# Kernel optimization log

Hardware: AMD Instinct MI355X
Metric: run time of the kernel (lower is better)

The kernel has to match this reference:

```python
import jax, jax.numpy as jnp
import numpy as np

EPS = 1e-8


def setup_inputs() -> dict:
    key = jax.random.key(0)
    k1, k2 = jax.random.split(key)
    N, D, K = 200000, 256, 64
    embeds = jax.random.normal(k1, (N, D), dtype=jnp.float32)
    init = jax.random.uniform(k2, (K, D), dtype=jnp.float32)  # torch.rand(K, n_h)
    beta = jnp.ones((1,), dtype=jnp.float32)
    return {"embeds": embeds, "init": init, "beta": beta, "num_iter": 11}


def reference(embeds, init, beta, num_iter):
    # embeds: [N, D], init: [K, D], beta: scalar temperature
    data_abs = jnp.linalg.norm(embeds, axis=1, keepdims=True)            # [N, 1]
    data_norm = embeds / jnp.maximum(data_abs, EPS)                      # [N, D]
    b = beta.reshape(())
    mu = init
    r = None
    for _ in range(num_iter):  # small fixed iteration count (default 11)
        mu_abs = jnp.linalg.norm(mu, axis=1, keepdims=True)              # [K, 1]
        mu_norm = mu / jnp.maximum(mu_abs, EPS)                          # [K, D]
        dist = data_norm @ mu_norm.T                                     # [N, K]
        r = jax.nn.softmax(b * dist, axis=1)                             # [N, K]
        cluster_r = r.sum(axis=0)                                        # [K]
        cluster_mean = r.T @ embeds                                      # [K, D]
        mu = cluster_mean / cluster_r[:, None]                           # diag(1/cluster_r) @ cluster_mean
    return mu, r
```

## Files before the change

kernel.cpp:

```cpp
#include <hip/hip_runtime.h>
#include <math.h>


#define N_ROWS 200000
#define DIM 256
#define KC 64
#define NUM_ITER 11
#define TR 64
#define NTILES (N_ROWS / TR)
#define EPSV 1e-8f
#define NB 256
#define NG2 8

typedef _Float16 half8 __attribute__((ext_vector_type(8)));
typedef _Float16 half4 __attribute__((ext_vector_type(4)));
typedef float f32x4 __attribute__((ext_vector_type(4)));

typedef __attribute__((address_space(3))) void as3_void;
typedef __attribute__((address_space(1))) void as1_void;

__device__ __forceinline__ void glds16(const void* g, void* l) {
  __builtin_amdgcn_global_load_lds((const as1_void*)g, (as3_void*)l, 16, 0, 0);
}

__device__ __forceinline__ float wave_reduce_sum(float v) {
#pragma unroll
  for (int off = 32; off > 0; off >>= 1) v += __shfl_xor(v, off, 64);
  return v;
}

__device__ __forceinline__ void barrier_lgkm_only() {
  __builtin_amdgcn_sched_barrier(0);
  asm volatile("s_waitcnt lgkmcnt(0)" ::: "memory");
  __builtin_amdgcn_s_barrier();
  __builtin_amdgcn_sched_barrier(0);
}


__global__ void rn_convert_kernel(const float* __restrict__ embeds,
                                  float* __restrict__ inv_norm,
                                  _Float16* __restrict__ Xh) {
  int gw = (blockIdx.x * blockDim.x + threadIdx.x) >> 6;
  int lane = threadIdx.x & 63;
  int nw = (gridDim.x * blockDim.x) >> 6;
  for (int row = gw; row < N_ROWS; row += nw) {
    float4 v = *(const float4*)(embeds + (size_t)row * DIM + 4 * lane);
    float s = v.x * v.x;
    s = fmaf(v.y, v.y, s); s = fmaf(v.z, v.z, s); s = fmaf(v.w, v.w, s);
    s = wave_reduce_sum(s);
    if (lane == 0) inv_norm[row] = 1.0f / fmaxf(sqrtf(s), EPSV);
    half4 h;
    h[0] = (_Float16)v.x; h[1] = (_Float16)v.y; h[2] = (_Float16)v.z; h[3] = (_Float16)v.w;
    *(half4*)(Xh + (size_t)row * DIM + 4 * lane) = h;
  }
}

__global__ void prep0f_kernel(const float* __restrict__ init,
                              _Float16* __restrict__ muh) {
  int k = blockIdx.x, lane = threadIdx.x;
  float4 v = *(const float4*)(init + (size_t)k * DIM + 4 * lane);
  float s = v.x * v.x;
  s = fmaf(v.y, v.y, s); s = fmaf(v.z, v.z, s); s = fmaf(v.w, v.w, s);
  s = wave_reduce_sum(s);
  float inv = 1.0f / fmaxf(sqrtf(s), EPSV);
  half4 h;
  h[0] = (_Float16)(v.x * inv); h[1] = (_Float16)(v.y * inv);
  h[2] = (_Float16)(v.z * inv); h[3] = (_Float16)(v.w * inv);
  *(half4*)(muh + (size_t)k * DIM + 4 * lane) = h;
}

__device__ __forceinline__ void stage_row512(const _Float16* g, _Float16* l,
                                             int wid, int lane) {
#pragma unroll
  for (int ii = 0; ii < 8; ++ii) {
    int i = wid * 8 + ii;
    int row = i * 2 + (lane >> 5);
    int slot = (lane & 31) ^ (row & 7);
    glds16((const char*)g + row * 512 + slot * 16, (char*)l + i * 1024);
  }
}

template <int LAST>
__global__ __launch_bounds__(256, 1) void cluster_main(
    const _Float16* __restrict__ Xh, const _Float16* __restrict__ muh,
    const float* __restrict__ inv_norm, const float* __restrict__ beta,
    float* __restrict__ part_cm, float* __restrict__ part_cr,
    float* __restrict__ r_out) {
  __shared__ alignas(16) _Float16 mu_lds[KC * DIM];
  __shared__ alignas(16) _Float16 x_lds[2][TR * DIM];
  __shared__ alignas(16) _Float16 xt_lds[DIM * TR];
  __shared__ alignas(16) _Float16 r_lds[KC * TR];
  __shared__ float cr_lds[4 * KC];

  const int tid = threadIdx.x, wid = tid >> 6, lane = tid & 63;
  const int l15 = lane & 15, h = lane >> 4;
  const float b = beta[0];
  const int myrow = 16 * wid + l15;

  const int rb0 = blockIdx.x;
  stage_row512(muh, mu_lds, wid, lane);
  stage_row512(Xh + (size_t)rb0 * TR * DIM, x_lds[0], wid, lane);

  f32x4 acc2[4][4] = {};
  float cr_acc[16] = {};
  __syncthreads();

  int p = 0;
  for (int rb = rb0; rb < NTILES; rb += NB, p ^= 1) {
    const int row0 = rb * TR;
    const int rbn = rb + NB;
    if (rbn < NTILES)
      stage_row512(Xh + (size_t)rbn * TR * DIM, x_lds[p ^ 1], wid, lane);

    f32x4 acc1[4] = {};
    const _Float16* xb = x_lds[p];
#pragma unroll
    for (int t = 0; t < 8; ++t) {
      const int kb = 32 * t + 8 * h;
      half8 bx = *(const half8*)&xb[myrow * DIM + (kb ^ ((myrow & 7) << 3))];
#pragma unroll
      for (int m = 0; m < 4; ++m) {
        const int cl = 16 * m + l15;
        half8 am = *(const half8*)&mu_lds[cl * DIM + (kb ^ ((cl & 7) << 3))];
        acc1[m] = __builtin_amdgcn_mfma_f32_16x16x32_f16(am, bx, acc1[m], 0, 0, 0);
      }
    }

    {
      const int db = tid >> 3;
      const int rb8 = tid & 7;
      union U { uint4 v; unsigned u[4]; };
      U tin[8];
#pragma unroll
      for (int k2 = 0; k2 < 8; ++k2)
        tin[k2].v = *(const uint4*)&xb[(8 * rb8 + k2) * DIM + ((8 * db) ^ (k2 << 3))];
#pragma unroll
      for (int j = 0; j < 8; ++j) {
        const unsigned sel = (j & 1) ? 0x07060302u : 0x05040100u;
        U o;
#pragma unroll
        for (int m2 = 0; m2 < 4; ++m2)
          o.u[m2] = __builtin_amdgcn_perm(tin[2 * m2 + 1].u[j >> 1],
                                          tin[2 * m2].u[j >> 1], sel);
        *(uint4*)&xt_lds[(8 * db + j) * TR + 8 * (rb8 ^ j)] = o.v;
      }
    }

    const int xr = row0 + myrow;
    const float sc = b * inv_norm[xr];
#pragma unroll
    for (int m = 0; m < 4; ++m)
#pragma unroll
      for (int j = 0; j < 4; ++j) acc1[m][j] *= sc;
    float mx = -1e30f;
#pragma unroll
    for (int m = 0; m < 4; ++m)
#pragma unroll
      for (int j = 0; j < 4; ++j) mx = fmaxf(mx, acc1[m][j]);
    mx = fmaxf(mx, __shfl_xor(mx, 16));
    mx = fmaxf(mx, __shfl_xor(mx, 32));
    float esum = 0.f;
#pragma unroll
    for (int m = 0; m < 4; ++m)
#pragma unroll
      for (int j = 0; j < 4; ++j) {
        float e = __expf(acc1[m][j] - mx);
        acc1[m][j] = e;
        esum += e;
      }
    esum += __shfl_xor(esum, 16);
    esum += __shfl_xor(esum, 32);
    const float rcp = 1.0f / esum;
#pragma unroll
    for (int m = 0; m < 4; ++m) {
#pragma unroll
      for (int j = 0; j < 4; ++j) {
        const float rv = acc1[m][j] * rcp;
        acc1[m][j] = rv;
        const int cl = 16 * m + 4 * h + j;
        cr_acc[m * 4 + j] += rv;
        r_lds[cl * TR + (myrow ^ ((cl & 7) << 3))] = (_Float16)rv;
      }
      if (LAST)
        *(float4*)&r_out[(size_t)xr * KC + 16 * m + 4 * h] = *(float4*)&acc1[m];
    }

    barrier_lgkm_only();

#pragma unroll
    for (int t = 0; t < 2; ++t) {
      const int kb = 32 * t + 8 * h;
      half8 ar[4], bx2[4];
#pragma unroll
      for (int m = 0; m < 4; ++m) {
        const int cl = 16 * m + l15;
        ar[m] = *(const half8*)&r_lds[cl * TR + (kb ^ ((cl & 7) << 3))];
      }
#pragma unroll
      for (int n = 0; n < 4; ++n) {
        const int dm = 64 * wid + 16 * n + l15;
        bx2[n] = *(const half8*)&xt_lds[dm * TR + (kb ^ ((dm & 7) << 3))];
      }
#pragma unroll
      for (int m = 0; m < 4; ++m)
#pragma unroll
        for (int n = 0; n < 4; ++n)
          acc2[m][n] = __builtin_amdgcn_mfma_f32_16x16x32_f16(ar[m], bx2[n], acc2[m][n], 0, 0, 0);
    }
    __syncthreads();
  }

  float* pc = part_cm + (size_t)blockIdx.x * (KC * DIM);
#pragma unroll
  for (int m = 0; m < 4; ++m)
#pragma unroll
    for (int n = 0; n < 4; ++n)
#pragma unroll
      for (int j = 0; j < 4; ++j)
        pc[(16 * m + 4 * h + j) * DIM + 64 * wid + 16 * n + l15] = acc2[m][n][j];
#pragma unroll
  for (int m = 0; m < 4; ++m)
#pragma unroll
    for (int j = 0; j < 4; ++j) {
      float v = cr_acc[m * 4 + j];
      v += __shfl_xor(v, 1); v += __shfl_xor(v, 2);
      v += __shfl_xor(v, 4); v += __shfl_xor(v, 8);
      if (l15 == 0) cr_lds[wid * KC + 16 * m + 4 * h + j] = v;
    }
  __syncthreads();
  if (wid == 0)
    part_cr[(size_t)blockIdx.x * KC + lane] =
        cr_lds[lane] + cr_lds[KC + lane] + cr_lds[2 * KC + lane] + cr_lds[3 * KC + lane];
}

__global__ void reduce_cm_kernel(const float* __restrict__ part_cm,
                                 float* __restrict__ part2) {
  const int k = blockIdx.x, g = blockIdx.y, t = threadIdx.x;
  float s = 0.f;
#pragma unroll
  for (int b = 0; b < NB / NG2; ++b)
    s += part_cm[(size_t)(g * (NB / NG2) + b) * (KC * DIM) + k * DIM + t];
  part2[(size_t)g * (KC * DIM) + k * DIM + t] = s;
}

template <int FINAL>
__global__ void norm_kernel(const float* __restrict__ part2,
                            const float* __restrict__ part_cr,
                            _Float16* __restrict__ muh,
                            float* __restrict__ mu_out) {
  const int k = blockIdx.x, t = threadIdx.x;
  __shared__ float red[256];
  red[t] = part_cr[(size_t)t * KC + k];
  __syncthreads();
#pragma unroll
  for (int off = 128; off > 0; off >>= 1) {
    if (t < off) red[t] += red[t + off];
    __syncthreads();
  }
  const float crv = red[0];
  __syncthreads();
  float s = 0.f;
#pragma unroll
  for (int g = 0; g < NG2; ++g) s += part2[(size_t)g * (KC * DIM) + k * DIM + t];
  const float mu = s / crv;
  if (FINAL) {
    mu_out[k * DIM + t] = mu;
    return;
  }
  red[t] = mu * mu;
  __syncthreads();
#pragma unroll
  for (int off = 128; off > 0; off >>= 1) {
    if (t < off) red[t] += red[t + off];
    __syncthreads();
  }
  const float inv = 1.0f / fmaxf(sqrtf(red[0]), EPSV);
  muh[k * DIM + t] = (_Float16)(mu * inv);
}

__global__ void rownorm_v1(const float* __restrict__ embeds, float* __restrict__ inv_norm) {
  int gw = (blockIdx.x * blockDim.x + threadIdx.x) >> 6;
  int lane = threadIdx.x & 63;
  int nw = (gridDim.x * blockDim.x) >> 6;
  for (int row = gw; row < N_ROWS; row += nw) {
    const float* rp = embeds + (size_t)row * DIM;
    float s = 0.f;
#pragma unroll
    for (int j = 0; j < 4; ++j) { float v = rp[lane + 64 * j]; s = fmaf(v, v, s); }
    s = wave_reduce_sum(s);
    if (lane == 0) inv_norm[row] = 1.0f / fmaxf(sqrtf(s), EPSV);
  }
}
__global__ void prep0_v1(const float* __restrict__ init, float* __restrict__ muT) {
  int k = blockIdx.x, lane = threadIdx.x;
  const float* rp = init + k * DIM;
  float v[4]; float s = 0.f;
#pragma unroll
  for (int j = 0; j < 4; ++j) { v[j] = rp[lane + 64 * j]; s = fmaf(v[j], v[j], s); }
  s = wave_reduce_sum(s);
  float inv = 1.0f / fmaxf(sqrtf(s), EPSV);
#pragma unroll
  for (int j = 0; j < 4; ++j) muT[(lane + 64 * j) * KC + k] = v[j] * inv;
}
__device__ __forceinline__ float wave_reduce_max_v1(float v) {
#pragma unroll
  for (int off = 32; off > 0; off >>= 1) v = fmaxf(v, __shfl_xor(v, off, 64));
  return v;
}
template <int LAST>
__global__ __launch_bounds__(256, 1) void main_v1(
    const float* __restrict__ embeds, const float* __restrict__ inv_norm,
    const float* __restrict__ muT, const float* __restrict__ beta,
    float* __restrict__ part_cm, float* __restrict__ part_cr,
    float* __restrict__ r_out, int nb) {
  __shared__ float mu_l[DIM * KC];
  __shared__ float x_l[TR * DIM];
  __shared__ float r_l[TR * KC];
  __shared__ float cr_l[4 * KC];
  const int tid = threadIdx.x, wid = tid >> 6, lane = tid & 63;
  const float b = beta[0];
  {
    const float4* m4 = (const float4*)muT; float4* ml4 = (float4*)mu_l;
#pragma unroll
    for (int i = 0; i < 16; ++i) ml4[tid + i * 256] = m4[tid + i * 256];
  }
  float acc[64];
#pragma unroll
  for (int i = 0; i < 64; ++i) acc[i] = 0.f;
  float cr = 0.f;
  for (int rb = blockIdx.x; rb < NTILES; rb += nb) {
    const int row0 = rb * TR;
    __syncthreads();
    {
      const float4* x4 = (const float4*)(embeds + (size_t)row0 * DIM);
      float4* xl4 = (float4*)x_l;
#pragma unroll
      for (int i = 0; i < 16; ++i) xl4[tid + i * 256] = x4[tid + i * 256];
    }
    __syncthreads();
    float dist[16];
#pragma unroll
    for (int r = 0; r < 16; ++r) dist[r] = 0.f;
    const int rbase = wid * 16;
    for (int d = 0; d < DIM; d += 4) {
      float mv0 = mu_l[(d + 0) * KC + lane], mv1 = mu_l[(d + 1) * KC + lane];
      float mv2 = mu_l[(d + 2) * KC + lane], mv3 = mu_l[(d + 3) * KC + lane];
#pragma unroll
      for (int r = 0; r < 16; ++r) {
        float4 xv = *(const float4*)&x_l[(rbase + r) * DIM + d];
        dist[r] = fmaf(xv.x, mv0, dist[r]); dist[r] = fmaf(xv.y, mv1, dist[r]);
        dist[r] = fmaf(xv.z, mv2, dist[r]); dist[r] = fmaf(xv.w, mv3, dist[r]);
      }
    }
#pragma unroll
    for (int r = 0; r < 16; ++r) {
      const int row = rbase + r;
      float s = b * (dist[r] * inv_norm[row0 + row]);
      float m = wave_reduce_max_v1(s);
      float e = __expf(s - m);
      float sum = wave_reduce_sum(e);
      float rv = e * (1.0f / sum);
      cr += rv;
      r_l[row * KC + lane] = rv;
      if (LAST) r_out[(size_t)(row0 + row) * KC + lane] = rv;
    }
    __syncthreads();
    const int dbase = wid * 64;
    for (int row = 0; row < TR; ++row) {
      float rv = r_l[row * KC + lane];
#pragma unroll
      for (int dd = 0; dd < 64; dd += 4) {
        float4 xv = *(const float4*)&x_l[row * DIM + dbase + dd];
        acc[dd + 0] = fmaf(rv, xv.x, acc[dd + 0]); acc[dd + 1] = fmaf(rv, xv.y, acc[dd + 1]);
        acc[dd + 2] = fmaf(rv, xv.z, acc[dd + 2]); acc[dd + 3] = fmaf(rv, xv.w, acc[dd + 3]);
      }
    }
  }
  {
    float* pp = part_cm + ((size_t)blockIdx.x * KC + lane) * DIM + wid * 64;
#pragma unroll
    for (int dd = 0; dd < 64; dd += 4)
      *(float4*)&pp[dd] = make_float4(acc[dd], acc[dd + 1], acc[dd + 2], acc[dd + 3]);
    cr_l[wid * KC + lane] = cr;
  }
  __syncthreads();
  if (wid == 0) {
    float c = cr_l[lane] + cr_l[64 + lane] + cr_l[128 + lane] + cr_l[192 + lane];
    part_cr[(size_t)blockIdx.x * KC + lane] = c;
  }
}
template <int FINAL>
__global__ void reduce_v1(const float* __restrict__ part_cm, const float* __restrict__ part_cr,
                          float* __restrict__ muT, float* __restrict__ mu_out, int nb) {
  const int k = blockIdx.x, t = threadIdx.x;
  __shared__ float red[256];
  float s = 0.f;
  for (int bl = 0; bl < nb; ++bl) s += part_cm[((size_t)bl * KC + k) * DIM + t];
  float c = 0.f;
  for (int bl = t; bl < nb; bl += 256) c += part_cr[(size_t)bl * KC + k];
  red[t] = c; __syncthreads();
#pragma unroll
  for (int off = 128; off > 0; off >>= 1) { if (t < off) red[t] += red[t + off]; __syncthreads(); }
  const float crv = red[0]; __syncthreads();
  const float mu = s / crv;
  if (FINAL) { mu_out[k * DIM + t] = mu; return; }
  red[t] = mu * mu; __syncthreads();
#pragma unroll
  for (int off = 128; off > 0; off >>= 1) { if (t < off) red[t] += red[t + off]; __syncthreads(); }
  const float inv = 1.0f / fmaxf(sqrtf(red[0]), EPSV);
  muT[t * KC + k] = mu * inv;
}

extern "C" void kernel_launch(void* const* d_in, const int* in_sizes, int n_in,
                              void* d_out, int out_size, void* d_ws, size_t ws_size,
                              hipStream_t stream) {
  const float* embeds = (const float*)d_in[0];
  const float* init = (const float*)d_in[1];
  const float* beta = (const float*)d_in[2];
  float* out_mu = (float*)d_out;
  float* out_r = out_mu + KC * DIM;
  char* ws = (char*)d_ws;

  const size_t szX = (size_t)N_ROWS * DIM * 2;
  const size_t szInv = (size_t)N_ROWS * 4;
  const size_t szMu = (size_t)KC * DIM * 2;
  const size_t szPC = (size_t)NB * KC * DIM * 4;
  const size_t szPR = (size_t)NB * KC * 4;
  const size_t szP2 = (size_t)NG2 * KC * DIM * 4;
  const size_t need = szX + szInv + szMu + szPC + szPR + szP2;

  if (ws_size >= need) {
    _Float16* Xh = (_Float16*)ws;
    float* invn = (float*)(ws + szX);
    _Float16* muh = (_Float16*)(ws + szX + szInv);
    float* pcm = (float*)(ws + szX + szInv + szMu);
    float* pcr = (float*)(ws + szX + szInv + szMu + szPC);
    float* p2 = (float*)(ws + szX + szInv + szMu + szPC + szPR);

    rn_convert_kernel<<<2048, 256, 0, stream>>>(embeds, invn, Xh);
    prep0f_kernel<<<KC, 64, 0, stream>>>(init, muh);
    for (int it = 0; it < NUM_ITER; ++it) {
      if (it > 0) {
        reduce_cm_kernel<<<dim3(KC, NG2), 256, 0, stream>>>(pcm, p2);
        norm_kernel<0><<<KC, 256, 0, stream>>>(p2, pcr, muh, nullptr);
      }
      if (it == NUM_ITER - 1)
        cluster_main<1><<<NB, 256, 0, stream>>>(Xh, muh, invn, beta, pcm, pcr, out_r);
      else
        cluster_main<0><<<NB, 256, 0, stream>>>(Xh, muh, invn, beta, pcm, pcr, out_r);
    }
    reduce_cm_kernel<<<dim3(KC, NG2), 256, 0, stream>>>(pcm, p2);
    norm_kernel<1><<<KC, 256, 0, stream>>>(p2, pcr, nullptr, out_mu);
  } else {
    float* wsf = (float*)d_ws;
    float* muT = wsf;
    float* invn = muT + DIM * KC;
    size_t avail = ws_size / sizeof(float);
    size_t fixed = (size_t)DIM * KC + N_ROWS;
    size_t per_blk = (size_t)KC * DIM + KC;
    int nb = 256;
    if (avail > fixed) {
      size_t mx = (avail - fixed) / per_blk;
      if (mx < 256) nb = (int)mx;
    } else nb = 1;
    if (nb < 1) nb = 1;
    float* pcm = invn + N_ROWS;
    float* pcr = pcm + (size_t)nb * KC * DIM;

    rownorm_v1<<<2048, 256, 0, stream>>>(embeds, invn);
    prep0_v1<<<KC, 64, 0, stream>>>(init, muT);
    for (int it = 0; it < NUM_ITER; ++it) {
      if (it > 0) reduce_v1<0><<<KC, 256, 0, stream>>>(pcm, pcr, muT, nullptr, nb);
      if (it == NUM_ITER - 1)
        main_v1<1><<<nb, 256, 0, stream>>>(embeds, invn, muT, beta, pcm, pcr, out_r, nb);
      else
        main_v1<0><<<nb, 256, 0, stream>>>(embeds, invn, muT, beta, pcm, pcr, nullptr, nb);
    }
    reduce_v1<1><<<KC, 256, 0, stream>>>(pcm, pcr, muT, out_mu, nb);
  }
}
```

Before: 581.4 us.

## Fuse all iterations into one persistent kernel with software grid barriers

Replaces the per-iteration launches of cluster_main, reduce_cm and norm with a single persistent kernel of 256 blocks. Atomic-counter grid barriers separate the phases, and each block reduces one quarter-row of the cluster means between barriers. Each block also prefetches its first X tile before the barrier and rebuilds normalized mu in LDS itself. This removes about 33 kernel launches and their gaps, but relies on all 256 blocks being co-resident and adds spin-wait barrier overhead.

```diff
diff --git a/kernel.cpp b/kernel.cpp
--- a/kernel.cpp
+++ b/kernel.cpp
@@ -10,7 +10,6 @@
 #define NTILES (N_ROWS / TR)
 #define EPSV 1e-8f
 #define NB 256
-#define NG2 8
 
 typedef _Float16 half8 __attribute__((ext_vector_type(8)));
 typedef _Float16 half4 __attribute__((ext_vector_type(4)));
@@ -34,6 +33,16 @@
   asm volatile("s_waitcnt lgkmcnt(0)" ::: "memory");
   __builtin_amdgcn_s_barrier();
   __builtin_amdgcn_sched_barrier(0);
+}
+
+__device__ __forceinline__ void grid_barrier(unsigned* bar) {
+  __syncthreads();
+  if (threadIdx.x == 0) {
+    __hip_atomic_fetch_add(bar, 1u, __ATOMIC_RELEASE, __HIP_MEMORY_SCOPE_AGENT);
+    while (__hip_atomic_load(bar, __ATOMIC_ACQUIRE, __HIP_MEMORY_SCOPE_AGENT) < NB)
+      __builtin_amdgcn_s_sleep(2);
+  }
+  __syncthreads();
 }
 
 
@@ -55,18 +64,17 @@
   }
 }
 
-__global__ void prep0f_kernel(const float* __restrict__ init,
-                              _Float16* __restrict__ muh) {
+__global__ void prep0_raw(const float* __restrict__ init, float* __restrict__ mu_raw,
+                          float* __restrict__ mu_ssq, unsigned* __restrict__ bars) {
   int k = blockIdx.x, lane = threadIdx.x;
   float4 v = *(const float4*)(init + (size_t)k * DIM + 4 * lane);
+  *(float4*)(mu_raw + (size_t)k * DIM + 4 * lane) = v;
   float s = v.x * v.x;
   s = fmaf(v.y, v.y, s); s = fmaf(v.z, v.z, s); s = fmaf(v.w, v.w, s);
-  s = wave_reduce_sum(s);
-  float inv = 1.0f / fmaxf(sqrtf(s), EPSV);
-  half4 h;
-  h[0] = (_Float16)(v.x * inv); h[1] = (_Float16)(v.y * inv);
-  h[2] = (_Float16)(v.z * inv); h[3] = (_Float16)(v.w * inv);
-  *(half4*)(muh + (size_t)k * DIM + 4 * lane) = h;
+#pragma unroll
+  for (int off = 1; off < 16; off <<= 1) s += __shfl_xor(s, off, 64);
+  if ((lane & 15) == 0) mu_ssq[k * 4 + (lane >> 4)] = s;
+  if (k == 0 && lane < 32) bars[lane] = 0;
 }
 
 __device__ __forceinline__ void stage_row512(const _Float16* g, _Float16* l,
@@ -80,202 +88,219 @@
   }
 }
 
-template <int LAST>
-__global__ __launch_bounds__(256, 1) void cluster_main(
-    const _Float16* __restrict__ Xh, const _Float16* __restrict__ muh,
-    const float* __restrict__ inv_norm, const float* __restrict__ beta,
-    float* __restrict__ part_cm, float* __restrict__ part_cr,
-    float* __restrict__ r_out) {
+__global__ __launch_bounds__(256, 1) void cluster_persist(
+    const _Float16* __restrict__ Xh, const float* __restrict__ inv_norm,
+    const float* __restrict__ beta, float* mu_raw, float* mu_ssq,
+    float* part_cm, float* part_crt, unsigned* bars,
+    float* __restrict__ r_out, float* __restrict__ mu_out) {
   __shared__ alignas(16) _Float16 mu_lds[KC * DIM];
   __shared__ alignas(16) _Float16 x_lds[2][TR * DIM];
   __shared__ alignas(16) _Float16 xt_lds[DIM * TR];
   __shared__ alignas(16) _Float16 r_lds[KC * TR];
   __shared__ float cr_lds[4 * KC];
+  __shared__ float red2[4 * 64];
+  __shared__ float cr4_lds[4];
 
   const int tid = threadIdx.x, wid = tid >> 6, lane = tid & 63;
   const int l15 = lane & 15, h = lane >> 4;
   const float b = beta[0];
   const int myrow = 16 * wid + l15;
-
   const int rb0 = blockIdx.x;
-  stage_row512(muh, mu_lds, wid, lane);
+
   stage_row512(Xh + (size_t)rb0 * TR * DIM, x_lds[0], wid, lane);
 
-  f32x4 acc2[4][4] = {};
-  float cr_acc[16] = {};
-  __syncthreads();
-
-  int p = 0;
-  for (int rb = rb0; rb < NTILES; rb += NB, p ^= 1) {
-    const int row0 = rb * TR;
-    const int rbn = rb + NB;
-    if (rbn < NTILES)
-      stage_row512(Xh + (size_t)rbn * TR * DIM, x_lds[p ^ 1], wid, lane);
-
-    f32x4 acc1[4] = {};
-    const _Float16* xb = x_lds[p];
-#pragma unroll
-    for (int t = 0; t < 8; ++t) {
-      const int kb = 32 * t + 8 * h;
-      half8 bx = *(const half8*)&xb[myrow * DIM + (kb ^ ((myrow & 7) << 3))];
+  for (int it = 0; it < NUM_ITER; ++it) {
+    const bool last = (it == NUM_ITER - 1);
+
+    if (tid < KC) {
+      const float4 s4 = *(const float4*)&mu_ssq[4 * tid];
+      cr_lds[tid] = 1.0f / fmaxf(sqrtf(s4.x + s4.y + s4.z + s4.w), EPSV);
+    }
+    __syncthreads();
+    {
+      const float4* mu_raw4 = (const float4*)mu_raw;
+#pragma unroll
+      for (int i = 0; i < 16; ++i) {
+        const int idx = tid + 256 * i;
+        const int cl = idx >> 6;
+        const int dim0 = (idx & 63) * 4;
+        float4 v = mu_raw4[idx];
+        const float iv = cr_lds[cl];
+        const int sw = dim0 ^ ((cl & 7) << 3);
+        half4 hh;
+        hh[0] = (_Float16)(v.x * iv); hh[1] = (_Float16)(v.y * iv);
+        hh[2] = (_Float16)(v.z * iv); hh[3] = (_Float16)(v.w * iv);
+        *(half4*)&mu_lds[cl * DIM + sw] = hh;
+      }
+    }
+    __syncthreads();
+
+    f32x4 acc2[4][4] = {};
+    float cr_acc[16] = {};
+    int p = 0;
+    for (int rb = rb0; rb < NTILES; rb += NB, p ^= 1) {
+      const int row0 = rb * TR;
+      const int rbn = rb + NB;
+      if (rbn < NTILES)
+        stage_row512(Xh + (size_t)rbn * TR * DIM, x_lds[p ^ 1], wid, lane);
+
+      f32x4 acc1[4] = {};
+      const _Float16* xb = x_lds[p];
+#pragma unroll
+      for (int t = 0; t < 8; ++t) {
+        const int kb = 32 * t + 8 * h;
+        half8 bx = *(const half8*)&xb[myrow * DIM + (kb ^ ((myrow & 7) << 3))];
+#pragma unroll
+        for (int m = 0; m < 4; ++m) {
+          const int cl = 16 * m + l15;
+          half8 am = *(const half8*)&mu_lds[cl * DIM + (kb ^ ((cl & 7) << 3))];
+          acc1[m] = __builtin_amdgcn_mfma_f32_16x16x32_f16(am, bx, acc1[m], 0, 0, 0);
+        }
+      }
+
+      {
+        const int db = tid >> 3;
+        const int rb8 = tid & 7;
+        union U { uint4 v; unsigned u[4]; };
+        U tin[8];
+#pragma unroll
+        for (int k2 = 0; k2 < 8; ++k2)
+          tin[k2].v = *(const uint4*)&xb[(8 * rb8 + k2) * DIM + ((8 * db) ^ (k2 << 3))];
+#pragma unroll
+        for (int j = 0; j < 8; ++j) {
+          const unsigned sel = (j & 1) ? 0x07060302u : 0x05040100u;
+          U o;
+#pragma unroll
+          for (int m2 = 0; m2 < 4; ++m2)
+            o.u[m2] = __builtin_amdgcn_perm(tin[2 * m2 + 1].u[j >> 1],
+                                            tin[2 * m2].u[j >> 1], sel);
+          *(uint4*)&xt_lds[(8 * db + j) * TR + 8 * (rb8 ^ j)] = o.v;
+        }
+      }
+
+      const int xr = row0 + myrow;
+      const float sc = b * inv_norm[xr];
+#pragma unroll
+      for (int m = 0; m < 4; ++m)
+#pragma unroll
+        for (int j = 0; j < 4; ++j) acc1[m][j] *= sc;
+      float mx = -1e30f;
+#pragma unroll
+      for (int m = 0; m < 4; ++m)
+#pragma unroll
+        for (int j = 0; j < 4; ++j) mx = fmaxf(mx, acc1[m][j]);
+      mx = fmaxf(mx, __shfl_xor(mx, 16));
+      mx = fmaxf(mx, __shfl_xor(mx, 32));
+      float esum = 0.f;
+#pragma unroll
+      for (int m = 0; m < 4; ++m)
+#pragma unroll
+        for (int j = 0; j < 4; ++j) {
+          float e = __expf(acc1[m][j] - mx);
+          acc1[m][j] = e;
+          esum += e;
+        }
+      esum += __shfl_xor(esum, 16);
+      esum += __shfl_xor(esum, 32);
+      const float rcp = 1.0f / esum;
 #pragma unroll
       for (int m = 0; m < 4; ++m) {
-        const int cl = 16 * m + l15;
-        half8 am = *(const half8*)&mu_lds[cl * DIM + (kb ^ ((cl & 7) << 3))];
-        acc1[m] = __builtin_amdgcn_mfma_f32_16x16x32_f16(am, bx, acc1[m], 0, 0, 0);
-      }
+#pragma unroll
+        for (int j = 0; j < 4; ++j) {
+          const float rv = acc1[m][j] * rcp;
+          acc1[m][j] = rv;
+          const int cl = 16 * m + 4 * h + j;
+          cr_acc[m * 4 + j] += rv;
+          r_lds[cl * TR + (myrow ^ ((cl & 7) << 3))] = (_Float16)rv;
+        }
+        if (last)
+          *(float4*)&r_out[(size_t)xr * KC + 16 * m + 4 * h] = *(float4*)&acc1[m];
+      }
+
+      barrier_lgkm_only();
+
+#pragma unroll
+      for (int t = 0; t < 2; ++t) {
+        const int kb = 32 * t + 8 * h;
+        half8 ar[4], bx2[4];
+#pragma unroll
+        for (int m = 0; m < 4; ++m) {
+          const int cl = 16 * m + l15;
+          ar[m] = *(const half8*)&r_lds[cl * TR + (kb ^ ((cl & 7) << 3))];
+        }
+#pragma unroll
+        for (int n = 0; n < 4; ++n) {
+          const int dm = 64 * wid + 16 * n + l15;
+          bx2[n] = *(const half8*)&xt_lds[dm * TR + (kb ^ ((dm & 7) << 3))];
+        }
+#pragma unroll
+        for (int m = 0; m < 4; ++m)
+#pragma unroll
+          for (int n = 0; n < 4; ++n)
+            acc2[m][n] = __builtin_amdgcn_mfma_f32_16x16x32_f16(ar[m], bx2[n], acc2[m][n], 0, 0, 0);
+      }
+      __syncthreads();
     }
 
     {
-      const int db = tid >> 3;
-      const int rb8 = tid & 7;
-      union U { uint4 v; unsigned u[4]; };
-      U tin[8];
-#pragma unroll
-      for (int k2 = 0; k2 < 8; ++k2)
-        tin[k2].v = *(const uint4*)&xb[(8 * rb8 + k2) * DIM + ((8 * db) ^ (k2 << 3))];
-#pragma unroll
-      for (int j = 0; j < 8; ++j) {
-        const unsigned sel = (j & 1) ? 0x07060302u : 0x05040100u;
-        U o;
-#pragma unroll
-        for (int m2 = 0; m2 < 4; ++m2)
-          o.u[m2] = __builtin_amdgcn_perm(tin[2 * m2 + 1].u[j >> 1],
-                                          tin[2 * m2].u[j >> 1], sel);
-        *(uint4*)&xt_lds[(8 * db + j) * TR + 8 * (rb8 ^ j)] = o.v;
-      }
-    }
-
-    const int xr = row0 + myrow;
-    const float sc = b * inv_norm[xr];
-#pragma unroll
-    for (int m = 0; m < 4; ++m)
-#pragma unroll
-      for (int j = 0; j < 4; ++j) acc1[m][j] *= sc;
-    float mx = -1e30f;
-#pragma unroll
-    for (int m = 0; m < 4; ++m)
-#pragma unroll
-      for (int j = 0; j < 4; ++j) mx = fmaxf(mx, acc1[m][j]);
-    mx = fmaxf(mx, __shfl_xor(mx, 16));
-    mx = fmaxf(mx, __shfl_xor(mx, 32));
-    float esum = 0.f;
-#pragma unroll
-    for (int m = 0; m < 4; ++m)
-#pragma unroll
-      for (int j = 0; j < 4; ++j) {
-        float e = __expf(acc1[m][j] - mx);
-        acc1[m][j] = e;
-        esum += e;
-      }
-    esum += __shfl_xor(esum, 16);
-    esum += __shfl_xor(esum, 32);
-    const float rcp = 1.0f / esum;
-#pragma unroll
-    for (int m = 0; m < 4; ++m) {
-#pragma unroll
-      for (int j = 0; j < 4; ++j) {
-        const float rv = acc1[m][j] * rcp;
-        acc1[m][j] = rv;
-        const int cl = 16 * m + 4 * h + j;
-        cr_acc[m * 4 + j] += rv;
-        r_lds[cl * TR + (myrow ^ ((cl & 7) << 3))] = (_Float16)rv;
-      }
-      if (LAST)
-        *(float4*)&r_out[(size_t)xr * KC + 16 * m + 4 * h] = *(float4*)&acc1[m];
-    }
-
-    barrier_lgkm_only();
-
-#pragma unroll
-    for (int t = 0; t < 2; ++t) {
-      const int kb = 32 * t + 8 * h;
-      half8 ar[4], bx2[4];
-#pragma unroll
-      for (int m = 0; m < 4; ++m) {
-        const int cl = 16 * m + l15;
-        ar[m] = *(const half8*)&r_lds[cl * TR + (kb ^ ((cl & 7) << 3))];
-      }
-#pragma unroll
-      for (int n = 0; n < 4; ++n) {
-        const int dm = 64 * wid + 16 * n + l15;
-        bx2[n] = *(const half8*)&xt_lds[dm * TR + (kb ^ ((dm & 7) << 3))];
-      }
+      float* pc = part_cm + (size_t)blockIdx.x * (KC * DIM);
 #pragma unroll
       for (int m = 0; m < 4; ++m)
 #pragma unroll
         for (int n = 0; n < 4; ++n)
-          acc2[m][n] = __builtin_amdgcn_mfma_f32_16x16x32_f16(ar[m], bx2[n], acc2[m][n], 0, 0, 0);
-    }
-    __syncthreads();
-  }
-
-  float* pc = part_cm + (size_t)blockIdx.x * (KC * DIM);
-#pragma unroll
-  for (int m = 0; m < 4; ++m)
-#pragma unroll
-    for (int n = 0; n < 4; ++n)
-#pragma unroll
-      for (int j = 0; j < 4; ++j)
-        pc[(16 * m + 4 * h + j) * DIM + 64 * wid + 16 * n + l15] = acc2[m][n][j];
-#pragma unroll
-  for (int m = 0; m < 4; ++m)
-#pragma unroll
-    for (int j = 0; j < 4; ++j) {
-      float v = cr_acc[m * 4 + j];
-      v += __shfl_xor(v, 1); v += __shfl_xor(v, 2);
-      v += __shfl_xor(v, 4); v += __shfl_xor(v, 8);
-      if (l15 == 0) cr_lds[wid * KC + 16 * m + 4 * h + j] = v;
-    }
-  __syncthreads();
-  if (wid == 0)
-    part_cr[(size_t)blockIdx.x * KC + lane] =
-        cr_lds[lane] + cr_lds[KC + lane] + cr_lds[2 * KC + lane] + cr_lds[3 * KC + lane];
-}
-
-__global__ void reduce_cm_kernel(const float* __restrict__ part_cm,
-                                 float* __restrict__ part2) {
-  const int k = blockIdx.x, g = blockIdx.y, t = threadIdx.x;
-  float s = 0.f;
-#pragma unroll
-  for (int b = 0; b < NB / NG2; ++b)
-    s += part_cm[(size_t)(g * (NB / NG2) + b) * (KC * DIM) + k * DIM + t];
-  part2[(size_t)g * (KC * DIM) + k * DIM + t] = s;
-}
-
-template <int FINAL>
-__global__ void norm_kernel(const float* __restrict__ part2,
-                            const float* __restrict__ part_cr,
-                            _Float16* __restrict__ muh,
-                            float* __restrict__ mu_out) {
-  const int k = blockIdx.x, t = threadIdx.x;
-  __shared__ float red[256];
-  red[t] = part_cr[(size_t)t * KC + k];
-  __syncthreads();
-#pragma unroll
-  for (int off = 128; off > 0; off >>= 1) {
-    if (t < off) red[t] += red[t + off];
-    __syncthreads();
-  }
-  const float crv = red[0];
-  __syncthreads();
-  float s = 0.f;
-#pragma unroll
-  for (int g = 0; g < NG2; ++g) s += part2[(size_t)g * (KC * DIM) + k * DIM + t];
-  const float mu = s / crv;
-  if (FINAL) {
-    mu_out[k * DIM + t] = mu;
-    return;
-  }
-  red[t] = mu * mu;
-  __syncthreads();
-#pragma unroll
-  for (int off = 128; off > 0; off >>= 1) {
-    if (t < off) red[t] += red[t + off];
-    __syncthreads();
-  }
-  const float inv = 1.0f / fmaxf(sqrtf(red[0]), EPSV);
-  muh[k * DIM + t] = (_Float16)(mu * inv);
+#pragma unroll
+          for (int j = 0; j < 4; ++j)
+            pc[(16 * m + 4 * h + j) * DIM + 64 * wid + 16 * n + l15] = acc2[m][n][j];
+#pragma unroll
+      for (int m = 0; m < 4; ++m)
+#pragma unroll
+        for (int j = 0; j < 4; ++j) {
+          float v = cr_acc[m * 4 + j];
+          v += __shfl_xor(v, 1); v += __shfl_xor(v, 2);
+          v += __shfl_xor(v, 4); v += __shfl_xor(v, 8);
+          if (l15 == 0) cr_lds[wid * KC + 16 * m + 4 * h + j] = v;
+        }
+      __syncthreads();
+      if (wid == 0) {
+        float c = cr_lds[lane] + cr_lds[KC + lane] + cr_lds[2 * KC + lane] + cr_lds[3 * KC + lane];
+        part_crt[(size_t)lane * NB + blockIdx.x] = c;
+      }
+    }
+
+    if (!last) stage_row512(Xh + (size_t)rb0 * TR * DIM, x_lds[0], wid, lane);
+
+    grid_barrier(&bars[2 * it]);
+
+    {
+      const int cl = blockIdx.x >> 2;
+      const int q = blockIdx.x & 3;
+      float c = part_crt[(size_t)cl * NB + tid];
+      c = wave_reduce_sum(c);
+      if (lane == 0) cr4_lds[wid] = c;
+      float s = 0.f;
+      const float* basep =
+          part_cm + (size_t)(64 * wid) * (KC * DIM) + cl * DIM + 64 * q + lane;
+#pragma unroll 8
+      for (int i = 0; i < 64; ++i) s += basep[(size_t)i * (KC * DIM)];
+      red2[wid * 64 + lane] = s;
+      __syncthreads();
+      if (wid == 0) {
+        const float crv = cr4_lds[0] + cr4_lds[1] + cr4_lds[2] + cr4_lds[3];
+        const float st = red2[lane] + red2[64 + lane] + red2[128 + lane] + red2[192 + lane];
+        const float mu = st / crv;
+        const int dim = 64 * q + lane;
+        if (!last) {
+          mu_raw[cl * DIM + dim] = mu;
+          float ss = wave_reduce_sum(mu * mu);
+          if (lane == 0) mu_ssq[cl * 4 + q] = ss;
+        } else {
+          mu_out[cl * DIM + dim] = mu;
+        }
+      }
+    }
+
+    if (!last) grid_barrier(&bars[2 * it + 1]);
+  }
 }
 
 __global__ void rownorm_v1(const float* __restrict__ embeds, float* __restrict__ inv_norm) {
@@ -423,34 +448,27 @@
 
   const size_t szX = (size_t)N_ROWS * DIM * 2;
   const size_t szInv = (size_t)N_ROWS * 4;
-  const size_t szMu = (size_t)KC * DIM * 2;
+  const size_t szMuR = (size_t)KC * DIM * 4;
+  const size_t szSsq = (size_t)KC * 4 * 4;
   const size_t szPC = (size_t)NB * KC * DIM * 4;
-  const size_t szPR = (size_t)NB * KC * 4;
-  const size_t szP2 = (size_t)NG2 * KC * DIM * 4;
-  const size_t need = szX + szInv + szMu + szPC + szPR + szP2;
+  const size_t szPR = (size_t)KC * NB * 4;
+  const size_t szBar = 128;
+  const size_t need = szX + szInv + szMuR + szSsq + szPC + szPR + szBar;
 
   if (ws_size >= need) {
-    _Float16* Xh = (_Float16*)ws;
-    float* invn = (float*)(ws + szX);
-    _Float16* muh = (_Float16*)(ws + szX + szInv);
-    float* pcm = (float*)(ws + szX + szInv + szMu);
-    float* pcr = (float*)(ws + szX + szInv + szMu + szPC);
-    float* p2 = (float*)(ws + szX + szInv + szMu + szPC + szPR);
+    char* pp = ws;
+    _Float16* Xh = (_Float16*)pp; pp += szX;
+    float* invn = (float*)pp; pp += szInv;
+    float* mu_raw = (float*)pp; pp += szMuR;
+    float* mu_ssq = (float*)pp; pp += szSsq;
+    float* pcm = (float*)pp; pp += szPC;
+    float* pcrt = (float*)pp; pp += szPR;
+    unsigned* bars = (unsigned*)pp;
 
     rn_convert_kernel<<<2048, 256, 0, stream>>>(embeds, invn, Xh);
-    prep0f_kernel<<<KC, 64, 0, stream>>>(init, muh);
-    for (int it = 0; it < NUM_ITER; ++it) {
-      if (it > 0) {
-        reduce_cm_kernel<<<dim3(KC, NG2), 256, 0, stream>>>(pcm, p2);
-        norm_kernel<0><<<KC, 256, 0, stream>>>(p2, pcr, muh, nullptr);
-      }
-      if (it == NUM_ITER - 1)
-        cluster_main<1><<<NB, 256, 0, stream>>>(Xh, muh, invn, beta, pcm, pcr, out_r);
-      else
-        cluster_main<0><<<NB, 256, 0, stream>>>(Xh, muh, invn, beta, pcm, pcr, out_r);
-    }
-    reduce_cm_kernel<<<dim3(KC, NG2), 256, 0, stream>>>(pcm, p2);
-    norm_kernel<1><<<KC, 256, 0, stream>>>(p2, pcr, nullptr, out_mu);
+    prep0_raw<<<KC, 64, 0, stream>>>(init, mu_raw, mu_ssq, bars);
+    cluster_persist<<<NB, 256, 0, stream>>>(Xh, invn, beta, mu_raw, mu_ssq,
+                                            pcm, pcrt, bars, out_r, out_mu);
   } else {
     float* wsf = (float*)d_ws;
     float* muT = wsf;
```

Result: slower. 1.237 ms (+112.7%).
